# Performance work log

Hardware: AMD Instinct MI355X
Metric: run time of the kernel (lower is better)

Reference implementation:

```python
import jax, jax.numpy as jnp
import numpy as np
import math

B, S, D, H = 2, 2048, 1024, 16
DK = D // H


def setup_inputs() -> dict:
    key = jax.random.key(0)
    ks = jax.random.split(key, 12)
    std = 1.0 / math.sqrt(D)
    inp = {
        "query": jax.random.normal(ks[0], (B, S, D), jnp.float32),
        "key_": jax.random.normal(ks[1], (B, S, D), jnp.float32),
        "value": jax.random.normal(ks[2], (B, S, D), jnp.float32),
        # causal mask: True = masked out
        "attn_mask": jnp.triu(jnp.ones((S, S), jnp.bool_), k=1),
        "w_q": jax.random.uniform(ks[3], (D, D), jnp.float32, -std, std),
        "b_q": jax.random.uniform(ks[4], (D,), jnp.float32, -std, std),
        "w_k": jax.random.uniform(ks[5], (D, D), jnp.float32, -std, std),
        "b_k": jax.random.uniform(ks[6], (D,), jnp.float32, -std, std),
        "w_v": jax.random.uniform(ks[7], (D, D), jnp.float32, -std, std),
        "b_v": jax.random.uniform(ks[8], (D,), jnp.float32, -std, std),
        "w_o": jax.random.uniform(ks[9], (D, D), jnp.float32, -std, std),
        "b_o": jax.random.uniform(ks[10], (D,), jnp.float32, -std, std),
    }
    return inp


def reference(query, key_, value, attn_mask, w_q, b_q, w_k, b_k, w_v, b_v, w_o, b_o):
    # linear projections (torch Linear: x @ W.T + b)
    q = query @ w_q.T + b_q
    k = key_ @ w_k.T + b_k
    v = value @ w_v.T + b_v
    # [B, H, S, DK]
    q = q.reshape(B, S, H, DK).transpose(0, 2, 1, 3)
    k = k.reshape(B, S, H, DK).transpose(0, 2, 1, 3)
    v = v.reshape(B, S, H, DK).transpose(0, 2, 1, 3)
    scores = jnp.einsum("bhqd,bhkd->bhqk", q, k) / jnp.sqrt(jnp.float32(DK))
    scores = jnp.where(attn_mask[None, None, :, :], -jnp.inf, scores)
    attn = jax.nn.softmax(scores, axis=-1)
    context = jnp.einsum("bhqk,bhkd->bhqd", attn, v)
    context = context.transpose(0, 2, 1, 3).reshape(B, S, D)
    return context @ w_o.T + b_o
```

## Files before the change

kernel.cpp:

```cpp
#include <hip/hip_runtime.h>

#define B_ 2
#define S_ 2048
#define D_ 1024
#define H_ 16
#define DK_ 64
#define K_ 1024

typedef __bf16 bf16x8 __attribute__((ext_vector_type(8)));
typedef __bf16 bf16x4 __attribute__((ext_vector_type(4)));
typedef float f32x4 __attribute__((ext_vector_type(4)));

#define QSCALE 0.18033688011112042f

__device__ __forceinline__ void gload16(const void* g, void* l) {
    __builtin_amdgcn_global_load_lds(
        (const __attribute__((address_space(1))) unsigned int*)g,
        (__attribute__((address_space(3))) unsigned int*)l, 16, 0, 0);
}

__device__ __forceinline__ bf16x8 cvt8f(const float* __restrict__ p) {
    f32x4 a = *reinterpret_cast<const f32x4*>(p);
    f32x4 b = *reinterpret_cast<const f32x4*>(p + 4);
    bf16x8 r;
#pragma unroll
    for (int j = 0; j < 4; ++j) { r[j] = (__bf16)a[j]; r[j + 4] = (__bf16)b[j]; }
    return r;
}

__global__ __launch_bounds__(256) void cvt3(
    const float* __restrict__ s0, const float* __restrict__ s1, const float* __restrict__ s2,
    __bf16* __restrict__ d0, __bf16* __restrict__ d1, __bf16* __restrict__ d2, int n8)
{
    const float* s; __bf16* d;
    if (blockIdx.y == 0) { s = s0; d = d0; }
    else if (blockIdx.y == 1) { s = s1; d = d1; }
    else { s = s2; d = d2; }
    int i = blockIdx.x * 256 + threadIdx.x;
    if (i >= n8) return;
    *reinterpret_cast<bf16x8*>(d + (size_t)i * 8) = cvt8f(s + (size_t)i * 8);
}

__global__ __launch_bounds__(256) void cvt4(
    const float* __restrict__ s0, const float* __restrict__ s1,
    const float* __restrict__ s2, const float* __restrict__ s3,
    __bf16* __restrict__ d0, __bf16* __restrict__ d1,
    __bf16* __restrict__ d2, __bf16* __restrict__ d3, int n8)
{
    const float* s; __bf16* d;
    if (blockIdx.y == 0) { s = s0; d = d0; }
    else if (blockIdx.y == 1) { s = s1; d = d1; }
    else if (blockIdx.y == 2) { s = s2; d = d2; }
    else { s = s3; d = d3; }
    int i = blockIdx.x * 256 + threadIdx.x;
    if (i >= n8) return;
    *reinterpret_cast<bf16x8*>(d + (size_t)i * 8) = cvt8f(s + (size_t)i * 8);
}

__device__ __forceinline__ void gemm_body_dbuf(
    const char* __restrict__ Ab, const char* __restrict__ Bb,
    int brow, int bcol, __bf16* ldsA, __bf16* ldsB, f32x4 (&acc)[4][4])
{
    const int tid = threadIdx.x;
    const int w = tid >> 6, lane = tid & 63;
    const int l15 = lane & 15, lh = lane >> 4;
    const int wr = w >> 1, wc = w & 1;
    const int srow  = lane >> 2;
    const int scolb = (lane & 3) * 16;

    auto stage = [&](int buf, int k0) {
#pragma unroll
        for (int c = 0; c < 2; ++c) {
            const int chunk = w * 2 + c;
            const int row   = chunk * 16 + srow;
            const int loff  = __builtin_amdgcn_readfirstlane(buf * 8192 + chunk * 1024);
            gload16(Ab + (size_t)(brow + row) * 2048 + k0 * 2 + scolb, (char*)ldsA + loff);
            gload16(Bb + (size_t)(bcol + row) * 2048 + k0 * 2 + scolb, (char*)ldsB + loff);
        }
    };

    stage(0, 0);
    int buf = 0;
    for (int k0 = 0; k0 < K_; k0 += 32) {
        if (k0 + 32 < K_) {
            stage(buf ^ 1, k0 + 32);
            asm volatile("s_waitcnt vmcnt(4)" ::: "memory");
        } else {
            asm volatile("s_waitcnt vmcnt(0)" ::: "memory");
        }
        __builtin_amdgcn_s_barrier();
        __builtin_amdgcn_sched_barrier(0);

        const int bo = buf * 4096;
        bf16x8 af[4], bfr[4];
#pragma unroll
        for (int m = 0; m < 4; ++m)
            af[m] = *reinterpret_cast<const bf16x8*>(&ldsA[bo + (wr * 64 + m * 16 + l15) * 32 + lh * 8]);
#pragma unroll
        for (int n = 0; n < 4; ++n)
            bfr[n] = *reinterpret_cast<const bf16x8*>(&ldsB[bo + (wc * 64 + n * 16 + l15) * 32 + lh * 8]);

        __builtin_amdgcn_s_setprio(1);
#pragma unroll
        for (int m = 0; m < 4; ++m)
#pragma unroll
            for (int n = 0; n < 4; ++n)
                acc[m][n] = __builtin_amdgcn_mfma_f32_16x16x32_bf16(af[m], bfr[n], acc[m][n], 0, 0, 0);
        __builtin_amdgcn_s_setprio(0);

        __builtin_amdgcn_s_barrier();
        buf ^= 1;
    }
}

__global__ __launch_bounds__(256) void gemm_qkv(
    const __bf16* __restrict__ qin, const __bf16* __restrict__ kin, const __bf16* __restrict__ vin,
    const __bf16* __restrict__ wq,  const __bf16* __restrict__ wk,  const __bf16* __restrict__ wv,
    const float* __restrict__ bq,   const float* __restrict__ bk,   const float* __restrict__ bv,
    __bf16* __restrict__ qo, __bf16* __restrict__ ko, __bf16* __restrict__ vto)
{
    __shared__ __attribute__((aligned(16))) __bf16 ldsA[2 * 128 * 32];
    __shared__ __attribute__((aligned(16))) __bf16 ldsB[2 * 128 * 32];

    const int z = blockIdx.z;
    const __bf16* A; const __bf16* Bm; const float* bias;
    int brow, bcol;
    if (z == 0)      { A = qin; Bm = wq; bias = bq; brow = blockIdx.x * 128; bcol = blockIdx.y * 128; }
    else if (z == 1) { A = kin; Bm = wk; bias = bk; brow = blockIdx.x * 128; bcol = blockIdx.y * 128; }
    else             { A = wv;  Bm = vin; bias = bv;
                       brow = (blockIdx.x & 7) * 128;
                       bcol = (blockIdx.y * 4 + (blockIdx.x >> 3)) * 128; }

    f32x4 acc[4][4] = {};
    gemm_body_dbuf((const char*)A, (const char*)Bm, brow, bcol, ldsA, ldsB, acc);

    const int tid = threadIdx.x;
    const int w = tid >> 6, lane = tid & 63;
    const int l15 = lane & 15, lh = lane >> 4;
    const int wr = w >> 1, wc = w & 1;

#pragma unroll
    for (int ni = 0; ni < 4; ++ni) {
        const int n = bcol + wc * 64 + ni * 16 + l15;
#pragma unroll
        for (int mi = 0; mi < 4; ++mi)
#pragma unroll
            for (int r = 0; r < 4; ++r) {
                const int m = brow + wr * 64 + mi * 16 + lh * 4 + r;
                if (z < 2) {
                    float v = acc[mi][ni][r] + bias[n];
                    if (z == 0) v *= QSCALE;
                    const int bb = m >> 11, ss = m & (S_ - 1);
                    const int hh = n >> 6,  dk = n & 63;
                    __bf16* o = (z == 0) ? qo : ko;
                    o[(((size_t)(bb * H_ + hh)) * S_ + ss) * DK_ + dk] = (__bf16)v;
                } else {
                    const float v = acc[mi][ni][r] + bias[m];
                    const int hh = m >> 6,  dk = m & 63;
                    const int bb = n >> 11, ss = n & (S_ - 1);
                    vto[(((size_t)(bb * H_ + hh)) * DK_ + dk) * S_ + ss] = (__bf16)v;
                }
            }
    }
}

__global__ __launch_bounds__(256) void gemm_out(
    const __bf16* __restrict__ A, const __bf16* __restrict__ Bm,
    const float* __restrict__ bias, float* __restrict__ out)
{
    __shared__ __attribute__((aligned(16))) __bf16 ldsA[2 * 128 * 32];
    __shared__ __attribute__((aligned(16))) __bf16 ldsB[2 * 128 * 32];

    const int brow = blockIdx.x * 128;
    const int bcol = blockIdx.y * 128;

    f32x4 acc[4][4] = {};
    gemm_body_dbuf((const char*)A, (const char*)Bm, brow, bcol, ldsA, ldsB, acc);

    const int tid = threadIdx.x;
    const int w = tid >> 6, lane = tid & 63;
    const int l15 = lane & 15, lh = lane >> 4;
    const int wr = w >> 1, wc = w & 1;

#pragma unroll
    for (int ni = 0; ni < 4; ++ni) {
        const int n = bcol + wc * 64 + ni * 16 + l15;
        const float bv = bias[n];
#pragma unroll
        for (int mi = 0; mi < 4; ++mi)
#pragma unroll
            for (int r = 0; r < 4; ++r) {
                const int m = brow + wr * 64 + mi * 16 + lh * 4 + r;
                out[(size_t)m * D_ + n] = acc[mi][ni][r] + bv;
            }
    }
}

__global__ __launch_bounds__(256, 4) void attn_kernel(
    const __bf16* __restrict__ Q, const __bf16* __restrict__ K,
    const __bf16* __restrict__ VT, __bf16* __restrict__ CTX)
{
    __shared__ __attribute__((aligned(16))) char ldsK[2][8192];
    __shared__ __attribute__((aligned(16))) char ldsV[2][8192];
    __shared__ __attribute__((aligned(16))) __bf16 p_lds[4][16][64];

    const int tid = threadIdx.x;
    const int w = tid >> 6, l = tid & 63;
    const int l15 = l & 15, lh = l >> 4;

    const int panel = 31 - (int)(blockIdx.x >> 5);
    const int bhidx = blockIdx.x & 31;
    const int h = bhidx & 15;
    const int b = bhidx >> 4;

    const size_t bh = (size_t)(b * H_ + h);
    const __bf16* qp   = Q + bh * S_ * DK_;
    const char*  kbase = (const char*)(K  + bh * S_ * DK_);
    const char*  vbase = (const char*)(VT + bh * DK_ * S_);

    const int np = panel + 1;
    const int wave_base = panel * 64 + w * 16;

    const int srow = l >> 3;
    const int ssw  = ((l & 7) * 16) ^ (srow * 16);

    auto stage = [&](int pos) {
        const int k0 = pos * 64;
        char* lk = ldsK[pos & 1];
        char* lv = ldsV[pos & 1];
#pragma unroll
        for (int i = 0; i < 2; ++i) {
            const int r0   = w * 16 + i * 8;
            const int loff = __builtin_amdgcn_readfirstlane(r0 * 128);
            gload16(kbase + (size_t)(k0 + r0 + srow) * 128 + ssw, lk + loff);
            gload16(vbase + (size_t)(r0 + srow) * 4096 + (size_t)k0 * 2 + ssw, lv + loff);
        }
    };

    bf16x8 aq[2];
#pragma unroll
    for (int c = 0; c < 2; ++c)
        aq[c] = *reinterpret_cast<const bf16x8*>(
            qp + (size_t)(wave_base + l15) * DK_ + c * 32 + lh * 8);

    f32x4 acc[4] = {};
    float mrun = -INFINITY, lrun = 0.f;

    stage(0);

    for (int it = 0; it < np; ++it) {
        if (it + 1 < np) {
            stage(it + 1);
            asm volatile("s_waitcnt vmcnt(4)" ::: "memory");
        } else {
            asm volatile("s_waitcnt vmcnt(0)" ::: "memory");
        }
        __builtin_amdgcn_s_barrier();
        __builtin_amdgcn_sched_barrier(0);

        const int k0 = it * 64;
        const char* lk = ldsK[it & 1];
        const char* lv = ldsV[it & 1];

        bf16x8 ak[4][2];
#pragma unroll
        for (int t = 0; t < 4; ++t)
#pragma unroll
            for (int c = 0; c < 2; ++c) {
                const int col = (c * 64 + lh * 16) ^ ((l15 & 7) << 4);
                ak[t][c] = *reinterpret_cast<const bf16x8*>(lk + (t * 16 + l15) * 128 + col);
            }

        f32x4 sacc[4] = {};
        __builtin_amdgcn_s_setprio(1);
#pragma unroll
        for (int t = 0; t < 4; ++t)
#pragma unroll
            for (int c = 0; c < 2; ++c)
                sacc[t] = __builtin_amdgcn_mfma_f32_16x16x32_bf16(
                    ak[t][c], aq[c], sacc[t], 0, 0, 0);
        __builtin_amdgcn_s_setprio(0);

        bf16x8 bv[4][2];
#pragma unroll
        for (int nt = 0; nt < 4; ++nt)
#pragma unroll
            for (int c2 = 0; c2 < 2; ++c2) {
                const int col = (c2 * 64 + lh * 16) ^ ((l15 & 7) << 4);
                bv[nt][c2] = *reinterpret_cast<const bf16x8*>(lv + (nt * 16 + l15) * 128 + col);
            }

        const bool domask = (k0 + 63 > wave_base);

        const int qa = wave_base + l15;
        float sc[4][4];
#pragma unroll
        for (int t = 0; t < 4; ++t)
#pragma unroll
            for (int r = 0; r < 4; ++r) {
                float s = sacc[t][r];
                if (domask) {
                    const int ka = k0 + t * 16 + lh * 4 + r;
                    s = (ka > qa) ? -INFINITY : s;
                }
                sc[t][r] = s;
            }
        float rm = sc[0][0];
#pragma unroll
        for (int t = 0; t < 4; ++t)
#pragma unroll
            for (int r = 0; r < 4; ++r) rm = fmaxf(rm, sc[t][r]);
        rm = fmaxf(rm, __shfl_xor(rm, 16, 64));
        rm = fmaxf(rm, __shfl_xor(rm, 32, 64));

        if (!__all(rm <= mrun + 8.f)) {
            const float mnew = fmaxf(mrun, rm);
            const float scl  = exp2f(mrun - mnew);
            mrun = mnew;
            lrun *= scl;
#pragma unroll
            for (int r = 0; r < 4; ++r) {
                const float sr = __shfl(scl, lh * 4 + r, 64);
#pragma unroll
                for (int nt = 0; nt < 4; ++nt) acc[nt][r] *= sr;
            }
        }

        float rs = 0.f;
#pragma unroll
        for (int t = 0; t < 4; ++t) {
            bf16x4 pk;
#pragma unroll
            for (int r = 0; r < 4; ++r) {
                const float p = exp2f(sc[t][r] - mrun);
                rs += p;
                pk[r] = (__bf16)p;
            }
            const int wcol = (t * 16 + lh * 4) ^ ((l15 & 7) << 3);
            *reinterpret_cast<bf16x4*>(&p_lds[w][l15][wcol]) = pk;
        }
        rs += __shfl_xor(rs, 16, 64);
        rs += __shfl_xor(rs, 32, 64);
        lrun += rs;

        bf16x8 pa[2];
#pragma unroll
        for (int c2 = 0; c2 < 2; ++c2) {
            const int rcol = (c2 * 32 + lh * 8) ^ ((l15 & 7) << 3);
            pa[c2] = *reinterpret_cast<const bf16x8*>(&p_lds[w][l15][rcol]);
        }

        __builtin_amdgcn_s_setprio(1);
#pragma unroll
        for (int nt = 0; nt < 4; ++nt)
#pragma unroll
            for (int c2 = 0; c2 < 2; ++c2)
                acc[nt] = __builtin_amdgcn_mfma_f32_16x16x32_bf16(
                    pa[c2], bv[nt][c2], acc[nt], 0, 0, 0);
        __builtin_amdgcn_s_setprio(0);

        __builtin_amdgcn_s_barrier();
    }

#pragma unroll
    for (int r = 0; r < 4; ++r) {
        const float linv = 1.f / __shfl(lrun, lh * 4 + r, 64);
        const int srow2 = wave_base + lh * 4 + r;
#pragma unroll
        for (int nt = 0; nt < 4; ++nt)
            CTX[((size_t)b * S_ + srow2) * D_ + h * DK_ + nt * 16 + l15] =
                (__bf16)(acc[nt][r] * linv);
    }
}

extern "C" void kernel_launch(void* const* d_in, const int* in_sizes, int n_in,
                              void* d_out, int out_size, void* d_ws, size_t ws_size,
                              hipStream_t stream) {
    (void)in_sizes; (void)n_in; (void)out_size; (void)ws_size;

    const float* query = (const float*)d_in[0];
    const float* key_  = (const float*)d_in[1];
    const float* value = (const float*)d_in[2];
    const float* w_q = (const float*)d_in[4];
    const float* b_q = (const float*)d_in[5];
    const float* w_k = (const float*)d_in[6];
    const float* b_k = (const float*)d_in[7];
    const float* w_v = (const float*)d_in[8];
    const float* b_v = (const float*)d_in[9];
    const float* w_o = (const float*)d_in[10];
    const float* b_o = (const float*)d_in[11];
    float* out = (float*)d_out;

    char* Wp = (char*)d_ws;
    const size_t MB = 1024 * 1024;
    __bf16* qin = (__bf16*)(Wp + 0 * MB);
    __bf16* kin = (__bf16*)(Wp + 8 * MB);
    __bf16* vin = (__bf16*)(Wp + 16 * MB);
    __bf16* wq  = (__bf16*)(Wp + 24 * MB);
    __bf16* wk  = (__bf16*)(Wp + 26 * MB);
    __bf16* wv  = (__bf16*)(Wp + 28 * MB);
    __bf16* wo  = (__bf16*)(Wp + 30 * MB);
    __bf16* q   = (__bf16*)(Wp + 32 * MB);
    __bf16* k   = (__bf16*)(Wp + 40 * MB);
    __bf16* vt  = (__bf16*)(Wp + 48 * MB);
    __bf16* ctx = qin;

    const int n8_big = (B_ * S_ * D_) / 8;
    const int n8_w   = (D_ * D_) / 8;

    hipLaunchKernelGGL(cvt3, dim3(n8_big / 256, 3), dim3(256), 0, stream,
                       query, key_, value, qin, kin, vin, n8_big);
    hipLaunchKernelGGL(cvt4, dim3(n8_w / 256, 4), dim3(256), 0, stream,
                       w_q, w_k, w_v, w_o, wq, wk, wv, wo, n8_w);
    hipLaunchKernelGGL(gemm_qkv, dim3(32, 8, 3), dim3(256), 0, stream,
                       qin, kin, vin, wq, wk, wv, b_q, b_k, b_v, q, k, vt);
    hipLaunchKernelGGL(attn_kernel, dim3(1024), dim3(256), 0, stream,
                       q, k, vt, ctx);
    hipLaunchKernelGGL(gemm_out, dim3(32, 8), dim3(256), 0, stream,
                       ctx, wo, b_o, out);
}
```

Baseline: 135.3 us.

## Use 256x256 tiled QKV GEMM with 4-stage LDS pipeline; compute softmax denominator via MFMA

Replaces the 128x128 double-buffered QKV projection GEMM with a 512-thread kernel computing 256x256 tiles. It uses a 4-deep LDS ring buffer with XOR-swizzled layout and prefetch two k-steps ahead, aiming for more operand reuse and fewer bank conflicts. The attention kernel drops the per-row shuffle reductions for the softmax sum and instead accumulates row sums with an extra MFMA against a ones vector. It also initializes score accumulators from a zero constant and simplifies masking. The larger tiles give only 192 blocks and 128KB of LDS per block, which may limit occupancy and load balance.

```diff
diff --git a/kernel.cpp b/kernel.cpp
--- a/kernel.cpp
+++ b/kernel.cpp
@@ -57,96 +57,103 @@
     *reinterpret_cast<bf16x8*>(d + (size_t)i * 8) = cvt8f(s + (size_t)i * 8);
 }
 
-__device__ __forceinline__ void gemm_body_dbuf(
-    const char* __restrict__ Ab, const char* __restrict__ Bb,
-    int brow, int bcol, __bf16* ldsA, __bf16* ldsB, f32x4 (&acc)[4][4])
-{
-    const int tid = threadIdx.x;
-    const int w = tid >> 6, lane = tid & 63;
-    const int l15 = lane & 15, lh = lane >> 4;
-    const int wr = w >> 1, wc = w & 1;
-    const int srow  = lane >> 2;
-    const int scolb = (lane & 3) * 16;
-
-    auto stage = [&](int buf, int k0) {
-#pragma unroll
-        for (int c = 0; c < 2; ++c) {
-            const int chunk = w * 2 + c;
-            const int row   = chunk * 16 + srow;
-            const int loff  = __builtin_amdgcn_readfirstlane(buf * 8192 + chunk * 1024);
-            gload16(Ab + (size_t)(brow + row) * 2048 + k0 * 2 + scolb, (char*)ldsA + loff);
-            gload16(Bb + (size_t)(bcol + row) * 2048 + k0 * 2 + scolb, (char*)ldsB + loff);
-        }
-    };
-
-    stage(0, 0);
-    int buf = 0;
-    for (int k0 = 0; k0 < K_; k0 += 32) {
-        if (k0 + 32 < K_) {
-            stage(buf ^ 1, k0 + 32);
-            asm volatile("s_waitcnt vmcnt(4)" ::: "memory");
-        } else {
-            asm volatile("s_waitcnt vmcnt(0)" ::: "memory");
-        }
-        __builtin_amdgcn_s_barrier();
-        __builtin_amdgcn_sched_barrier(0);
-
-        const int bo = buf * 4096;
-        bf16x8 af[4], bfr[4];
-#pragma unroll
-        for (int m = 0; m < 4; ++m)
-            af[m] = *reinterpret_cast<const bf16x8*>(&ldsA[bo + (wr * 64 + m * 16 + l15) * 32 + lh * 8]);
-#pragma unroll
-        for (int n = 0; n < 4; ++n)
-            bfr[n] = *reinterpret_cast<const bf16x8*>(&ldsB[bo + (wc * 64 + n * 16 + l15) * 32 + lh * 8]);
-
-        __builtin_amdgcn_s_setprio(1);
-#pragma unroll
-        for (int m = 0; m < 4; ++m)
-#pragma unroll
-            for (int n = 0; n < 4; ++n)
-                acc[m][n] = __builtin_amdgcn_mfma_f32_16x16x32_bf16(af[m], bfr[n], acc[m][n], 0, 0, 0);
-        __builtin_amdgcn_s_setprio(0);
-
-        __builtin_amdgcn_s_barrier();
-        buf ^= 1;
-    }
-}
-
-__global__ __launch_bounds__(256) void gemm_qkv(
+__global__ __launch_bounds__(512) void gemm_qkv256(
     const __bf16* __restrict__ qin, const __bf16* __restrict__ kin, const __bf16* __restrict__ vin,
     const __bf16* __restrict__ wq,  const __bf16* __restrict__ wk,  const __bf16* __restrict__ wv,
     const float* __restrict__ bq,   const float* __restrict__ bk,   const float* __restrict__ bv,
     __bf16* __restrict__ qo, __bf16* __restrict__ ko, __bf16* __restrict__ vto)
 {
-    __shared__ __attribute__((aligned(16))) __bf16 ldsA[2 * 128 * 32];
-    __shared__ __attribute__((aligned(16))) __bf16 ldsB[2 * 128 * 32];
-
-    const int z = blockIdx.z;
-    const __bf16* A; const __bf16* Bm; const float* bias;
-    int brow, bcol;
-    if (z == 0)      { A = qin; Bm = wq; bias = bq; brow = blockIdx.x * 128; bcol = blockIdx.y * 128; }
-    else if (z == 1) { A = kin; Bm = wk; bias = bk; brow = blockIdx.x * 128; bcol = blockIdx.y * 128; }
-    else             { A = wv;  Bm = vin; bias = bv;
-                       brow = (blockIdx.x & 7) * 128;
-                       bcol = (blockIdx.y * 4 + (blockIdx.x >> 3)) * 128; }
-
-    f32x4 acc[4][4] = {};
-    gemm_body_dbuf((const char*)A, (const char*)Bm, brow, bcol, ldsA, ldsB, acc);
+    __shared__ __attribute__((aligned(16))) char lds[4][32768];
 
     const int tid = threadIdx.x;
     const int w = tid >> 6, lane = tid & 63;
     const int l15 = lane & 15, lh = lane >> 4;
-    const int wr = w >> 1, wc = w & 1;
+    const int wr = w >> 2, wc = w & 3;
+
+    const int z = blockIdx.y;
+    const __bf16* A; const __bf16* Bm; const float* bias;
+    int brow, bcol;
+    if (z == 0)      { A = qin; Bm = wq;  bias = bq; brow = (blockIdx.x & 15) * 256; bcol = (blockIdx.x >> 4) * 256; }
+    else if (z == 1) { A = kin; Bm = wk;  bias = bk; brow = (blockIdx.x & 15) * 256; bcol = (blockIdx.x >> 4) * 256; }
+    else             { A = wv;  Bm = vin; bias = bv; brow = (blockIdx.x & 3)  * 256; bcol = (blockIdx.x >> 2) * 256; }
+
+    const char* Ab = (const char*)A;
+    const char* Bb = (const char*)Bm;
+
+    auto stageAB = [&](int tt, int p) {
+        char* base = lds[tt & 3];
+        const char* src = (p == 0) ? Ab : Bb;
+        const int rowbase = (p == 0) ? brow : bcol;
+        const int dsto = (p == 0) ? 0 : 16384;
+        const int koff = tt * 64;
+#pragma unroll
+        for (int j = 0; j < 2; ++j) {
+            const int s    = j * 512 + tid;
+            const int row  = s >> 2;
+            const int slot = s & 3;
+            const int scol = (slot ^ ((row >> 1) & 3)) * 16;
+            const int loff = __builtin_amdgcn_readfirstlane(dsto + (j * 512 + w * 64) * 16);
+            gload16(src + (size_t)(rowbase + row) * 2048 + koff + scol, base + loff);
+        }
+    };
+
+    auto readA = [&](int buf, int msub) -> bf16x8 {
+        const int hrow = wr * 128 + msub * 16 + l15;
+        const int off  = hrow * 64 + ((lh << 4) ^ ((hrow & 6) << 3));
+        return *reinterpret_cast<const bf16x8*>(&lds[buf][off]);
+    };
+    auto readB = [&](int buf, int nsub) -> bf16x8 {
+        const int hrow = wc * 64 + nsub * 16 + l15;
+        const int off  = 16384 + hrow * 64 + ((lh << 4) ^ ((hrow & 6) << 3));
+        return *reinterpret_cast<const bf16x8*>(&lds[buf][off]);
+    };
+
+    f32x4 acc[8][4] = {};
+    const int NT = K_ / 32;
+
+    stageAB(0, 0); stageAB(0, 1); stageAB(1, 0); stageAB(1, 1);
+    asm volatile("s_waitcnt vmcnt(4)" ::: "memory");
+    __builtin_amdgcn_s_barrier();
+
+    bf16x8 bfr[4];
+    for (int t = 0; t < NT; ++t) {
+        const int buf = t & 3;
+#pragma unroll
+        for (int p = 0; p < 2; ++p) {
+            bf16x8 af[4];
+#pragma unroll
+            for (int i = 0; i < 4; ++i) af[i] = readA(buf, p * 4 + i);
+            if (p == 0) {
+#pragma unroll
+                for (int n = 0; n < 4; ++n) bfr[n] = readB(buf, n);
+            }
+            if (t + 2 < NT) stageAB(t + 2, p);
+            if (p == 1) {
+                if (t < NT - 2)       { asm volatile("s_waitcnt vmcnt(4)" ::: "memory"); }
+                else if (t == NT - 2) { asm volatile("s_waitcnt vmcnt(0)" ::: "memory"); }
+            }
+            __builtin_amdgcn_s_barrier();
+            asm volatile("s_waitcnt lgkmcnt(0)" ::: "memory");
+            __builtin_amdgcn_sched_barrier(0);
+            __builtin_amdgcn_s_setprio(1);
+#pragma unroll
+            for (int i = 0; i < 4; ++i)
+#pragma unroll
+                for (int n = 0; n < 4; ++n)
+                    acc[p * 4 + i][n] = __builtin_amdgcn_mfma_f32_16x16x32_bf16(
+                        af[i], bfr[n], acc[p * 4 + i][n], 0, 0, 0);
+            __builtin_amdgcn_s_setprio(0);
+        }
+    }
 
 #pragma unroll
     for (int ni = 0; ni < 4; ++ni) {
         const int n = bcol + wc * 64 + ni * 16 + l15;
 #pragma unroll
-        for (int mi = 0; mi < 4; ++mi)
+        for (int mi = 0; mi < 8; ++mi)
 #pragma unroll
             for (int r = 0; r < 4; ++r) {
-                const int m = brow + wr * 64 + mi * 16 + lh * 4 + r;
+                const int m = brow + wr * 128 + mi * 16 + lh * 4 + r;
                 if (z < 2) {
                     float v = acc[mi][ni][r] + bias[n];
                     if (z == 0) v *= QSCALE;
@@ -164,6 +171,62 @@
     }
 }
 
+__device__ __forceinline__ void gemm_body_dbuf(
+    const char* __restrict__ Ab, const char* __restrict__ Bb,
+    int brow, int bcol, __bf16* ldsA, __bf16* ldsB, f32x4 (&acc)[4][4])
+{
+    const int tid = threadIdx.x;
+    const int w = tid >> 6, lane = tid & 63;
+    const int l15 = lane & 15, lh = lane >> 4;
+    const int wr = w >> 1, wc = w & 1;
+    const int srow  = lane >> 2;
+    const int scolb = (lane & 3) * 16;
+
+    auto stage = [&](int buf, int k0) {
+#pragma unroll
+        for (int c = 0; c < 2; ++c) {
+            const int chunk = w * 2 + c;
+            const int row   = chunk * 16 + srow;
+            const int loff  = __builtin_amdgcn_readfirstlane(buf * 8192 + chunk * 1024);
+            gload16(Ab + (size_t)(brow + row) * 2048 + k0 * 2 + scolb, (char*)ldsA + loff);
+            gload16(Bb + (size_t)(bcol + row) * 2048 + k0 * 2 + scolb, (char*)ldsB + loff);
+        }
+    };
+
+    stage(0, 0);
+    int buf = 0;
+    for (int k0 = 0; k0 < K_; k0 += 32) {
+        if (k0 + 32 < K_) {
+            stage(buf ^ 1, k0 + 32);
+            asm volatile("s_waitcnt vmcnt(4)" ::: "memory");
+        } else {
+            asm volatile("s_waitcnt vmcnt(0)" ::: "memory");
+        }
+        __builtin_amdgcn_s_barrier();
+        __builtin_amdgcn_sched_barrier(0);
+
+        const int bo = buf * 4096;
+        bf16x8 af[4], bfr[4];
+#pragma unroll
+        for (int m = 0; m < 4; ++m)
+            af[m] = *reinterpret_cast<const bf16x8*>(&ldsA[bo + (wr * 64 + m * 16 + l15) * 32 + lh * 8]);
+#pragma unroll
+        for (int n = 0; n < 4; ++n)
+            bfr[n] = *reinterpret_cast<const bf16x8*>(&ldsB[bo + (wc * 64 + n * 16 + l15) * 32 + lh * 8]);
+
+        __builtin_amdgcn_s_setprio(1);
+#pragma unroll
+        for (int m = 0; m < 4; ++m)
+#pragma unroll
+            for (int n = 0; n < 4; ++n)
+                acc[m][n] = __builtin_amdgcn_mfma_f32_16x16x32_bf16(af[m], bfr[n], acc[m][n], 0, 0, 0);
+        __builtin_amdgcn_s_setprio(0);
+
+        __builtin_amdgcn_s_barrier();
+        buf ^= 1;
+    }
+}
+
 __global__ __launch_bounds__(256) void gemm_out(
     const __bf16* __restrict__ A, const __bf16* __restrict__ Bm,
     const float* __restrict__ bias, float* __restrict__ out)
@@ -243,8 +306,14 @@
         aq[c] = *reinterpret_cast<const bf16x8*>(
             qp + (size_t)(wave_base + l15) * DK_ + c * 32 + lh * 8);
 
+    bf16x8 vones;
+#pragma unroll
+    for (int j = 0; j < 8; ++j) vones[j] = (__bf16)1.0f;
+    const f32x4 fzero = {0.f, 0.f, 0.f, 0.f};
+
     f32x4 acc[4] = {};
-    float mrun = -INFINITY, lrun = 0.f;
+    f32x4 acc_l = {};
+    float mrun = -INFINITY;
 
     stage(0);
 
@@ -271,14 +340,13 @@
                 ak[t][c] = *reinterpret_cast<const bf16x8*>(lk + (t * 16 + l15) * 128 + col);
             }
 
-        f32x4 sacc[4] = {};
+        f32x4 sacc[4];
         __builtin_amdgcn_s_setprio(1);
 #pragma unroll
-        for (int t = 0; t < 4; ++t)
-#pragma unroll
-            for (int c = 0; c < 2; ++c)
-                sacc[t] = __builtin_amdgcn_mfma_f32_16x16x32_bf16(
-                    ak[t][c], aq[c], sacc[t], 0, 0, 0);
+        for (int t = 0; t < 4; ++t) {
+            sacc[t] = __builtin_amdgcn_mfma_f32_16x16x32_bf16(ak[t][0], aq[0], fzero, 0, 0, 0);
+            sacc[t] = __builtin_amdgcn_mfma_f32_16x16x32_bf16(ak[t][1], aq[1], sacc[t], 0, 0, 0);
+        }
         __builtin_amdgcn_s_setprio(0);
 
         bf16x8 bv[4][2];
@@ -290,26 +358,23 @@
                 bv[nt][c2] = *reinterpret_cast<const bf16x8*>(lv + (nt * 16 + l15) * 128 + col);
             }
 
-        const bool domask = (k0 + 63 > wave_base);
-
-        const int qa = wave_base + l15;
-        float sc[4][4];
-#pragma unroll
-        for (int t = 0; t < 4; ++t)
-#pragma unroll
-            for (int r = 0; r < 4; ++r) {
-                float s = sacc[t][r];
-                if (domask) {
+        if (k0 + 63 > wave_base) {
+            const int qa = wave_base + l15;
+#pragma unroll
+            for (int t = 0; t < 4; ++t)
+#pragma unroll
+                for (int r = 0; r < 4; ++r) {
                     const int ka = k0 + t * 16 + lh * 4 + r;
-                    s = (ka > qa) ? -INFINITY : s;
+                    if (ka > qa) sacc[t][r] = -INFINITY;
                 }
-                sc[t][r] = s;
-            }
-        float rm = sc[0][0];
-#pragma unroll
-        for (int t = 0; t < 4; ++t)
-#pragma unroll
-            for (int r = 0; r < 4; ++r) rm = fmaxf(rm, sc[t][r]);
+        }
+
+        f32x4 m4 = sacc[0];
+#pragma unroll
+        for (int t = 1; t < 4; ++t)
+#pragma unroll
+            for (int r = 0; r < 4; ++r) m4[r] = fmaxf(m4[r], sacc[t][r]);
+        float rm = fmaxf(fmaxf(m4[0], m4[1]), fmaxf(m4[2], m4[3]));
         rm = fmaxf(rm, __shfl_xor(rm, 16, 64));
         rm = fmaxf(rm, __shfl_xor(rm, 32, 64));
 
@@ -317,31 +382,24 @@
             const float mnew = fmaxf(mrun, rm);
             const float scl  = exp2f(mrun - mnew);
             mrun = mnew;
-            lrun *= scl;
 #pragma unroll
             for (int r = 0; r < 4; ++r) {
                 const float sr = __shfl(scl, lh * 4 + r, 64);
 #pragma unroll
                 for (int nt = 0; nt < 4; ++nt) acc[nt][r] *= sr;
-            }
-        }
-
-        float rs = 0.f;
+                acc_l[r] *= sr;
+            }
+        }
+
 #pragma unroll
         for (int t = 0; t < 4; ++t) {
             bf16x4 pk;
 #pragma unroll
-            for (int r = 0; r < 4; ++r) {
-                const float p = exp2f(sc[t][r] - mrun);
-                rs += p;
-                pk[r] = (__bf16)p;
-            }
+            for (int r = 0; r < 4; ++r)
+                pk[r] = (__bf16)exp2f(sacc[t][r] - mrun);
             const int wcol = (t * 16 + lh * 4) ^ ((l15 & 7) << 3);
             *reinterpret_cast<bf16x4*>(&p_lds[w][l15][wcol]) = pk;
         }
-        rs += __shfl_xor(rs, 16, 64);
-        rs += __shfl_xor(rs, 32, 64);
-        lrun += rs;
 
         bf16x8 pa[2];
 #pragma unroll
@@ -357,6 +415,8 @@
             for (int c2 = 0; c2 < 2; ++c2)
                 acc[nt] = __builtin_amdgcn_mfma_f32_16x16x32_bf16(
                     pa[c2], bv[nt][c2], acc[nt], 0, 0, 0);
+        acc_l = __builtin_amdgcn_mfma_f32_16x16x32_bf16(pa[0], vones, acc_l, 0, 0, 0);
+        acc_l = __builtin_amdgcn_mfma_f32_16x16x32_bf16(pa[1], vones, acc_l, 0, 0, 0);
         __builtin_amdgcn_s_setprio(0);
 
         __builtin_amdgcn_s_barrier();
@@ -364,7 +424,7 @@
 
 #pragma unroll
     for (int r = 0; r < 4; ++r) {
-        const float linv = 1.f / __shfl(lrun, lh * 4 + r, 64);
+        const float linv = 1.f / acc_l[r];
         const int srow2 = wave_base + lh * 4 + r;
 #pragma unroll
         for (int nt = 0; nt < 4; ++nt)
@@ -412,7 +472,7 @@
                        query, key_, value, qin, kin, vin, n8_big);
     hipLaunchKernelGGL(cvt4, dim3(n8_w / 256, 4), dim3(256), 0, stream,
                        w_q, w_k, w_v, w_o, wq, wk, wv, wo, n8_w);
-    hipLaunchKernelGGL(gemm_qkv, dim3(32, 8, 3), dim3(256), 0, stream,
+    hipLaunchKernelGGL(gemm_qkv256, dim3(64, 3), dim3(512), 0, stream,
                        qin, kin, vin, wq, wk, wv, b_q, b_k, b_v, q, k, vt);
     hipLaunchKernelGGL(attn_kernel, dim3(1024), dim3(256), 0, stream,
                        q, k, vt, ctx);
```

Measured after the change: 134.6 us. Within noise of the previous version (-0.5%).
